# Kernel optimization log

Measured on AMD Instinct MI355X. Metric: run time of the kernel, lower is better.

The kernel has to match this reference:

```python
import jax, jax.numpy as jnp
import numpy as np

B, S, H = 32, 2048, 1024

def setup_inputs() -> dict:
    key = jax.random.key(0)
    ks = jax.random.split(key, 8)
    s = 1.0 / np.sqrt(H)
    return {
        "query": jax.random.normal(ks[0], (B, 1, H), jnp.float32),
        "keys": jax.random.normal(ks[1], (B, S, H), jnp.float32),
        "Wa_w": jax.random.normal(ks[2], (H, H), jnp.float32) * s,
        "Wa_b": jax.random.normal(ks[3], (H,), jnp.float32) * s,
        "Ua_w": jax.random.normal(ks[4], (H, H), jnp.float32) * s,
        "Ua_b": jax.random.normal(ks[5], (H,), jnp.float32) * s,
        "Va_w": jax.random.normal(ks[6], (1, H), jnp.float32) * s,
        "Va_b": jax.random.normal(ks[7], (1,), jnp.float32) * s,
    }

def reference(query, keys, Wa_w, Wa_b, Ua_w, Ua_b, Va_w, Va_b):
    # Wa(query): (B,1,H); Ua(keys): (B,S,H); broadcast add -> (B,S,H)
    q = jnp.einsum('bqh,oh->bqo', query, Wa_w) + Wa_b
    k = jnp.einsum('bsh,oh->bso', keys, Ua_w) + Ua_b
    h = jnp.tanh(q + k)                              # (B,S,H)
    scores = jnp.einsum('bsh,oh->bso', h, Va_w) + Va_b  # (B,S,1)
    scores = scores[:, :, 0][:, None, :]             # (B,1,S)
    weights = jax.nn.softmax(scores, axis=-1)        # (B,1,S)
    context = jnp.einsum('bqs,bsh->bqh', weights, keys)  # (B,1,H)
    return context, weights
```

## Files before the change

kernel.cpp:

```cpp
#include <hip/hip_runtime.h>
#include <hip/hip_bf16.h>

#define HDIM 1024
#define SEQ  2048
#define BATCH 32
#define M_TOTAL (BATCH * SEQ)
#define BM 256
#define BN 256
#define BK 32
#define KSTEPS (HDIM / BK)
#define NSLICE 16

typedef __bf16 bf16x8 __attribute__((ext_vector_type(8)));
typedef float  f32x4  __attribute__((ext_vector_type(4)));
typedef unsigned short u16;
#define AS1 __attribute__((address_space(1)))
#define AS3 __attribute__((address_space(3)))

__device__ __forceinline__ u16 f2bf(float f) {
    unsigned int u = __float_as_uint(f);
    u += 0x7FFFu + ((u >> 16) & 1u);
    return (u16)(u >> 16);
}

__global__ __launch_bounds__(256) void cvt_kernel(const float* __restrict__ in,
                                                  u16* __restrict__ out) {
    size_t i = ((size_t)blockIdx.x * 256 + threadIdx.x) * 8;
    float4 f0 = *(const float4*)(in + i);
    float4 f1 = *(const float4*)(in + i + 4);
    uint4 v;
    v.x = (unsigned)f2bf(f0.x) | ((unsigned)f2bf(f0.y) << 16);
    v.y = (unsigned)f2bf(f0.z) | ((unsigned)f2bf(f0.w) << 16);
    v.z = (unsigned)f2bf(f1.x) | ((unsigned)f2bf(f1.y) << 16);
    v.w = (unsigned)f2bf(f1.z) | ((unsigned)f2bf(f1.w) << 16);
    *(uint4*)(out + i) = v;
}

__global__ __launch_bounds__(256) void qb_kernel(const float* __restrict__ query,
                                                 const float* __restrict__ Wa_w,
                                                 const float* __restrict__ Wa_b,
                                                 const float* __restrict__ Ua_b,
                                                 float* __restrict__ qb) {
    __shared__ float qs[HDIM];
    const int b = blockIdx.x;
    const int tid = threadIdx.x;
    ((float4*)qs)[tid] = ((const float4*)(query + b * HDIM))[tid];
    __syncthreads();
    const int lane = tid & 63;
    const int w = tid >> 6;
    const int obase = blockIdx.y * 64 + w * 16;
    for (int i = 0; i < 16; i++) {
        int o = obase + i;
        const float4* wrow = (const float4*)(Wa_w + (size_t)o * HDIM);
        float s = 0.f;
        #pragma unroll
        for (int j = 0; j < 4; j++) {
            float4 wv = wrow[j * 64 + lane];
            float4 qv = ((const float4*)qs)[j * 64 + lane];
            s += wv.x * qv.x + wv.y * qv.y + wv.z * qv.z + wv.w * qv.w;
        }
        #pragma unroll
        for (int m = 1; m < 64; m <<= 1) s += __shfl_xor(s, m);
        if (lane == 0) qb[b * HDIM + o] = s + Wa_b[o] + Ua_b[o];
    }
}

#define DSREAD(dst, base, imm) \
    asm volatile("ds_read_b128 %0, %1 offset:" #imm : "=v"(dst) : "v"(base))

#define MFMA4(mi, av, b0v, b1v, b2v, b3v) \
    acc[mi][0] = __builtin_amdgcn_mfma_f32_16x16x32_bf16(av, b0v, acc[mi][0], 0, 0, 0); \
    acc[mi][1] = __builtin_amdgcn_mfma_f32_16x16x32_bf16(av, b1v, acc[mi][1], 0, 0, 0); \
    acc[mi][2] = __builtin_amdgcn_mfma_f32_16x16x32_bf16(av, b2v, acc[mi][2], 0, 0, 0); \
    acc[mi][3] = __builtin_amdgcn_mfma_f32_16x16x32_bf16(av, b3v, acc[mi][3], 0, 0, 0);

__global__ __launch_bounds__(512, 2) void gemm_score_kernel(const u16* __restrict__ keysb,
                                                            const u16* __restrict__ uab,
                                                            const float* __restrict__ qb,
                                                            const float* __restrict__ vaw,
                                                            float* __restrict__ sp) {
    __shared__ __align__(16) u16 As[4][BM * BK];
    __shared__ __align__(16) u16 Bs[4][BN * BK];

    const int tid  = threadIdx.x;
    const int lane = tid & 63;
    const int w    = tid >> 6;
    const int wm   = w >> 2;
    const int wn   = w & 3;

    const int bid = blockIdx.y * 4 + blockIdx.x;
    const int swz = (bid & 7) * 128 + (bid >> 3);
    const int bx  = swz & 3;
    const int by  = swz >> 2;
    const int n0  = bx * BN;
    const int m0  = by * BM;

    const int srow = lane >> 2;
    const int cs   = (lane & 3) ^ ((lane >> 3) & 3);
    const u16* gA0 = keysb + (size_t)(m0 + w * 32 + srow) * HDIM + cs * 8;
    const u16* gB0 = uab   + (size_t)(n0 + w * 32 + srow) * HDIM + cs * 8;
    const int ldst = w * 32 * BK;

    const int fr = lane & 15;
    const int fq = lane >> 4;
    const int sA = fq ^ ((fr >> 1) & 3);
    const unsigned aB0 = (unsigned)(unsigned long long)(const AS3 u16*)&As[0][0]
                       + (unsigned)(((wm * 128 + fr) * BK + sA * 8) * 2);
    const unsigned bB0 = (unsigned)(unsigned long long)(const AS3 u16*)&Bs[0][0]
                       + (unsigned)(((wn * 64  + fr) * BK + sA * 8) * 2);

    f32x4 acc[8][4] = {};

#define STAGE_A(kt) { \
    u16* d = &As[(kt) & 3][ldst]; \
    __builtin_amdgcn_global_load_lds((AS1 void*)(gA0 + (size_t)(kt) * BK), (AS3 void*)d, 16, 0, 0); \
    __builtin_amdgcn_global_load_lds((AS1 void*)(gA0 + (size_t)(kt) * BK + 16 * HDIM), (AS3 void*)(d + 16 * BK), 16, 0, 0); }
#define STAGE_B(kt) { \
    u16* d = &Bs[(kt) & 3][ldst]; \
    __builtin_amdgcn_global_load_lds((AS1 void*)(gB0 + (size_t)(kt) * BK), (AS3 void*)d, 16, 0, 0); \
    __builtin_amdgcn_global_load_lds((AS1 void*)(gB0 + (size_t)(kt) * BK + 16 * HDIM), (AS3 void*)(d + 16 * BK), 16, 0, 0); }

    bf16x8 a0, a1, a2, a3, a4, a5, a6, a7;
    bf16x8 bA0, bA1, bA2, bA3, bB0v, bB1v, bB2v, bB3v;

    STAGE_A(0) STAGE_B(0)
    STAGE_A(1) STAGE_B(1)
    STAGE_A(2) STAGE_B(2)
    asm volatile("s_waitcnt vmcnt(4)" ::: "memory");
    __builtin_amdgcn_s_barrier();
    DSREAD(a0, aB0, 0);    DSREAD(a1, aB0, 1024);
    DSREAD(a2, aB0, 2048); DSREAD(a3, aB0, 3072);
    DSREAD(bA0, bB0, 0);    DSREAD(bA1, bB0, 1024);
    DSREAD(bA2, bB0, 2048); DSREAD(bA3, bB0, 3072);

#define TILE(t, bc0, bc1, bc2, bc3, bn0, bn1, bn2, bn3) { \
    const unsigned at = aB0 + (((t) & 3) << 14);              \
     \
    if ((t) + 3 < KSTEPS) STAGE_A((t) + 3) \
    DSREAD(a4, at, 4096); DSREAD(a5, at, 5120); \
    DSREAD(a6, at, 6144); DSREAD(a7, at, 7168); \
    asm volatile("s_waitcnt lgkmcnt(4)" ::: "memory");        \
    __builtin_amdgcn_sched_barrier(0); \
    __builtin_amdgcn_s_setprio(1); \
    MFMA4(0, a0, bc0, bc1, bc2, bc3) \
    MFMA4(1, a1, bc0, bc1, bc2, bc3) \
    MFMA4(2, a2, bc0, bc1, bc2, bc3) \
    MFMA4(3, a3, bc0, bc1, bc2, bc3) \
    __builtin_amdgcn_s_setprio(0); \
     \
    if ((t) + 3 < KSTEPS) STAGE_B((t) + 3) \
    if ((t) + 1 < KSTEPS) { \
        const unsigned an = aB0 + ((((t) + 1) & 3) << 14); \
        const unsigned bn = bB0 + ((((t) + 1) & 3) << 14); \
        DSREAD(a0, an, 0);    DSREAD(a1, an, 1024); \
        DSREAD(a2, an, 2048); DSREAD(a3, an, 3072); \
        DSREAD(bn0, bn, 0);    DSREAD(bn1, bn, 1024); \
        DSREAD(bn2, bn, 2048); DSREAD(bn3, bn, 3072); \
        asm volatile("s_waitcnt lgkmcnt(8)" ::: "memory");    \
    } else { \
        asm volatile("s_waitcnt lgkmcnt(0)" ::: "memory"); \
    } \
    __builtin_amdgcn_sched_barrier(0); \
    __builtin_amdgcn_s_setprio(1); \
    MFMA4(4, a4, bc0, bc1, bc2, bc3) \
    MFMA4(5, a5, bc0, bc1, bc2, bc3) \
    MFMA4(6, a6, bc0, bc1, bc2, bc3) \
    MFMA4(7, a7, bc0, bc1, bc2, bc3) \
    __builtin_amdgcn_s_setprio(0); \
     \
    if ((t) + 1 < KSTEPS - 2) asm volatile("s_waitcnt vmcnt(4)" ::: "memory"); \
    else                      asm volatile("s_waitcnt vmcnt(0)" ::: "memory"); \
    __builtin_amdgcn_s_barrier(); \
}

    for (int t = 0; t < KSTEPS; t += 2) {
        TILE(t,     bA0, bA1, bA2, bA3, bB0v, bB1v, bB2v, bB3v)
        TILE(t + 1, bB0v, bB1v, bB2v, bB3v, bA0, bA1, bA2, bA3)
    }
#undef TILE
#undef STAGE_A
#undef STAGE_B

    const int bidx = m0 >> 11;
    float qv[4], vv[4];
    #pragma unroll
    for (int ni = 0; ni < 4; ni++) {
        int n_g = n0 + wn * 64 + ni * 16 + fr;
        qv[ni] = qb[bidx * HDIM + n_g];
        vv[ni] = vaw[n_g];
    }
    const int slice = bx * 4 + wn;
    float* sl = sp + ((size_t)slice * BATCH + bidx) * SEQ;
    #pragma unroll
    for (int mi = 0; mi < 8; mi++) {
        #pragma unroll
        for (int r = 0; r < 4; r++) {
            float p = 0.f;
            #pragma unroll
            for (int ni = 0; ni < 4; ni++) {
                float x = acc[mi][ni][r] + qv[ni];
                float e = __expf(2.f * x);
                p += (1.f - 2.f / (e + 1.f)) * vv[ni];
            }
            p += __shfl_xor(p, 1);
            p += __shfl_xor(p, 2);
            p += __shfl_xor(p, 4);
            p += __shfl_xor(p, 8);
            if (fr == 0) {
                int s_g = (m0 + wm * 128 + mi * 16 + fq * 4 + r) & (SEQ - 1);
                sl[s_g] = p;
            }
        }
    }
}

__global__ __launch_bounds__(256) void softmax_kernel(const float* __restrict__ sp,
                                                      float* __restrict__ weights,
                                                      float* __restrict__ ctx) {
    __shared__ float red[4];
    const int b = blockIdx.x;
    const int tid = threadIdx.x;
    float4 z = {0.f, 0.f, 0.f, 0.f};
    ((float4*)(ctx + b * HDIM))[tid] = z;
    float v[8];
    float mx = -1e30f;
    #pragma unroll
    for (int i = 0; i < 8; i++) {
        int s = tid + i * 256;
        float a = 0.f;
        #pragma unroll
        for (int j = 0; j < NSLICE; j++) a += sp[((size_t)j * BATCH + b) * SEQ + s];
        v[i] = a;
        mx = fmaxf(mx, a);
    }
    #pragma unroll
    for (int m = 1; m < 64; m <<= 1) mx = fmaxf(mx, __shfl_xor(mx, m));
    if ((tid & 63) == 0) red[tid >> 6] = mx;
    __syncthreads();
    mx = fmaxf(fmaxf(red[0], red[1]), fmaxf(red[2], red[3]));
    float sum = 0.f;
    #pragma unroll
    for (int i = 0; i < 8; i++) { v[i] = __expf(v[i] - mx); sum += v[i]; }
    #pragma unroll
    for (int m = 1; m < 64; m <<= 1) sum += __shfl_xor(sum, m);
    __syncthreads();
    if ((tid & 63) == 0) red[tid >> 6] = sum;
    __syncthreads();
    sum = red[0] + red[1] + red[2] + red[3];
    float inv = 1.f / sum;
    #pragma unroll
    for (int i = 0; i < 8; i++) weights[b * SEQ + tid + i * 256] = v[i] * inv;
}

__global__ __launch_bounds__(256) void context_kernel(const u16* __restrict__ keysb,
                                                      const float* __restrict__ weights,
                                                      float* __restrict__ ctx) {
    __shared__ float wsm[256];
    const int b = blockIdx.x;
    const int s0 = blockIdx.y * 256;
    const int tid = threadIdx.x;
    wsm[tid] = weights[b * SEQ + s0 + tid];
    __syncthreads();
    const int hq = tid & 127;
    const int sh = (tid >> 7) * 128;
    float a0 = 0.f, a1 = 0.f, a2 = 0.f, a3 = 0.f;
    float a4 = 0.f, a5 = 0.f, a6 = 0.f, a7 = 0.f;
    const uint4* kp = (const uint4*)(keysb + (size_t)b * SEQ * HDIM
                                     + (size_t)(s0 + sh) * HDIM) + hq;
    #pragma unroll 8
    for (int s = 0; s < 128; s++) {
        uint4 kv = kp[s * 128];
        float wv = wsm[sh + s];
        a0 += wv * __uint_as_float(kv.x << 16);
        a1 += wv * __uint_as_float(kv.x & 0xFFFF0000u);
        a2 += wv * __uint_as_float(kv.y << 16);
        a3 += wv * __uint_as_float(kv.y & 0xFFFF0000u);
        a4 += wv * __uint_as_float(kv.z << 16);
        a5 += wv * __uint_as_float(kv.z & 0xFFFF0000u);
        a6 += wv * __uint_as_float(kv.w << 16);
        a7 += wv * __uint_as_float(kv.w & 0xFFFF0000u);
    }
    float* o = ctx + b * HDIM + hq * 8;
    atomicAdd(o + 0, a0);
    atomicAdd(o + 1, a1);
    atomicAdd(o + 2, a2);
    atomicAdd(o + 3, a3);
    atomicAdd(o + 4, a4);
    atomicAdd(o + 5, a5);
    atomicAdd(o + 6, a6);
    atomicAdd(o + 7, a7);
}

extern "C" void kernel_launch(void* const* d_in, const int* in_sizes, int n_in,
                              void* d_out, int out_size, void* d_ws, size_t ws_size,
                              hipStream_t stream) {
    const float* query = (const float*)d_in[0];
    const float* keys  = (const float*)d_in[1];
    const float* Wa_w  = (const float*)d_in[2];
    const float* Wa_b  = (const float*)d_in[3];
    const float* Ua_w  = (const float*)d_in[4];
    const float* Ua_b  = (const float*)d_in[5];
    const float* Va_w  = (const float*)d_in[6];
    float* out = (float*)d_out;

    char* ws = (char*)d_ws;
    u16*  keysb = (u16*)ws;
    u16*  uab   = (u16*)(ws + 134217728);
    float* qb   = (float*)(ws + 134217728 + 2097152);
    float* sp   = (float*)(ws + 134217728 + 2097152 + 131072);

    cvt_kernel<<<(BATCH * SEQ * HDIM) / 2048, 256, 0, stream>>>(keys, keysb);
    cvt_kernel<<<(HDIM * HDIM) / 2048, 256, 0, stream>>>(Ua_w, uab);
    qb_kernel<<<dim3(BATCH, HDIM / 64), 256, 0, stream>>>(query, Wa_w, Wa_b, Ua_b, qb);
    gemm_score_kernel<<<dim3(HDIM / BN, M_TOTAL / BM), 512, 0, stream>>>(keysb, uab, qb, Va_w, sp);
    softmax_kernel<<<BATCH, 256, 0, stream>>>(sp, out + BATCH * HDIM, out);
    context_kernel<<<dim3(BATCH, 8), 256, 0, stream>>>(keysb, out + BATCH * HDIM, out);
}
```

Measured before the change: 598.6 us.

## Load GEMM B fragments directly from global, widen softmax/context blocks, grid-stride convert

```diff
diff --git a/kernel.cpp b/kernel.cpp
--- a/kernel.cpp
+++ b/kernel.cpp
@@ -24,16 +24,19 @@
 }
 
 __global__ __launch_bounds__(256) void cvt_kernel(const float* __restrict__ in,
-                                                  u16* __restrict__ out) {
-    size_t i = ((size_t)blockIdx.x * 256 + threadIdx.x) * 8;
-    float4 f0 = *(const float4*)(in + i);
-    float4 f1 = *(const float4*)(in + i + 4);
-    uint4 v;
-    v.x = (unsigned)f2bf(f0.x) | ((unsigned)f2bf(f0.y) << 16);
-    v.y = (unsigned)f2bf(f0.z) | ((unsigned)f2bf(f0.w) << 16);
-    v.z = (unsigned)f2bf(f1.x) | ((unsigned)f2bf(f1.y) << 16);
-    v.w = (unsigned)f2bf(f1.z) | ((unsigned)f2bf(f1.w) << 16);
-    *(uint4*)(out + i) = v;
+                                                  u16* __restrict__ out, int n8) {
+    const int stride = gridDim.x * 256;
+    for (int idx = blockIdx.x * 256 + threadIdx.x; idx < n8; idx += stride) {
+        size_t i = (size_t)idx * 8;
+        float4 f0 = *(const float4*)(in + i);
+        float4 f1 = *(const float4*)(in + i + 4);
+        uint4 v;
+        v.x = (unsigned)f2bf(f0.x) | ((unsigned)f2bf(f0.y) << 16);
+        v.y = (unsigned)f2bf(f0.z) | ((unsigned)f2bf(f0.w) << 16);
+        v.z = (unsigned)f2bf(f1.x) | ((unsigned)f2bf(f1.y) << 16);
+        v.w = (unsigned)f2bf(f1.z) | ((unsigned)f2bf(f1.w) << 16);
+        *(uint4*)(out + i) = v;
+    }
 }
 
 __global__ __launch_bounds__(256) void qb_kernel(const float* __restrict__ query,
@@ -68,11 +71,11 @@
 #define DSREAD(dst, base, imm) \
     asm volatile("ds_read_b128 %0, %1 offset:" #imm : "=v"(dst) : "v"(base))
 
-#define MFMA4(mi, av, b0v, b1v, b2v, b3v) \
-    acc[mi][0] = __builtin_amdgcn_mfma_f32_16x16x32_bf16(av, b0v, acc[mi][0], 0, 0, 0); \
-    acc[mi][1] = __builtin_amdgcn_mfma_f32_16x16x32_bf16(av, b1v, acc[mi][1], 0, 0, 0); \
-    acc[mi][2] = __builtin_amdgcn_mfma_f32_16x16x32_bf16(av, b2v, acc[mi][2], 0, 0, 0); \
-    acc[mi][3] = __builtin_amdgcn_mfma_f32_16x16x32_bf16(av, b3v, acc[mi][3], 0, 0, 0);
+#define MFMA4(mi, av, c0, c1, c2, c3) \
+    acc[mi][0] = __builtin_amdgcn_mfma_f32_16x16x32_bf16(av, c0, acc[mi][0], 0, 0, 0); \
+    acc[mi][1] = __builtin_amdgcn_mfma_f32_16x16x32_bf16(av, c1, acc[mi][1], 0, 0, 0); \
+    acc[mi][2] = __builtin_amdgcn_mfma_f32_16x16x32_bf16(av, c2, acc[mi][2], 0, 0, 0); \
+    acc[mi][3] = __builtin_amdgcn_mfma_f32_16x16x32_bf16(av, c3, acc[mi][3], 0, 0, 0);
 
 __global__ __launch_bounds__(512, 2) void gemm_score_kernel(const u16* __restrict__ keysb,
                                                             const u16* __restrict__ uab,
@@ -80,7 +83,6 @@
                                                             const float* __restrict__ vaw,
                                                             float* __restrict__ sp) {
     __shared__ __align__(16) u16 As[4][BM * BK];
-    __shared__ __align__(16) u16 Bs[4][BN * BK];
 
     const int tid  = threadIdx.x;
     const int lane = tid & 63;
@@ -98,7 +100,6 @@
     const int srow = lane >> 2;
     const int cs   = (lane & 3) ^ ((lane >> 3) & 3);
     const u16* gA0 = keysb + (size_t)(m0 + w * 32 + srow) * HDIM + cs * 8;
-    const u16* gB0 = uab   + (size_t)(n0 + w * 32 + srow) * HDIM + cs * 8;
     const int ldst = w * 32 * BK;
 
     const int fr = lane & 15;
@@ -106,8 +107,11 @@
     const int sA = fq ^ ((fr >> 1) & 3);
     const unsigned aB0 = (unsigned)(unsigned long long)(const AS3 u16*)&As[0][0]
                        + (unsigned)(((wm * 128 + fr) * BK + sA * 8) * 2);
-    const unsigned bB0 = (unsigned)(unsigned long long)(const AS3 u16*)&Bs[0][0]
-                       + (unsigned)(((wn * 64  + fr) * BK + sA * 8) * 2);
+    const AS1 u16* gBp0 = (const AS1 u16*)uab
+                        + ((size_t)(n0 + wn * 64 + fr) * HDIM + fq * 8);
+    const AS1 u16* gBp1 = gBp0 + (size_t)16 * HDIM;
+    const AS1 u16* gBp2 = gBp0 + (size_t)32 * HDIM;
+    const AS1 u16* gBp3 = gBp0 + (size_t)48 * HDIM;
 
     f32x4 acc[8][4] = {};
 
@@ -115,71 +119,70 @@
     u16* d = &As[(kt) & 3][ldst]; \
     __builtin_amdgcn_global_load_lds((AS1 void*)(gA0 + (size_t)(kt) * BK), (AS3 void*)d, 16, 0, 0); \
     __builtin_amdgcn_global_load_lds((AS1 void*)(gA0 + (size_t)(kt) * BK + 16 * HDIM), (AS3 void*)(d + 16 * BK), 16, 0, 0); }
-#define STAGE_B(kt) { \
-    u16* d = &Bs[(kt) & 3][ldst]; \
-    __builtin_amdgcn_global_load_lds((AS1 void*)(gB0 + (size_t)(kt) * BK), (AS3 void*)d, 16, 0, 0); \
-    __builtin_amdgcn_global_load_lds((AS1 void*)(gB0 + (size_t)(kt) * BK + 16 * HDIM), (AS3 void*)(d + 16 * BK), 16, 0, 0); }
 
     bf16x8 a0, a1, a2, a3, a4, a5, a6, a7;
-    bf16x8 bA0, bA1, bA2, bA3, bB0v, bB1v, bB2v, bB3v;
-
-    STAGE_A(0) STAGE_B(0)
-    STAGE_A(1) STAGE_B(1)
-    STAGE_A(2) STAGE_B(2)
+    bf16x8 bA0, bA1, bA2, bA3, bB0, bB1, bB2, bB3;
+
+    bA0 = *(const AS1 bf16x8*)(gBp0);
+    bA1 = *(const AS1 bf16x8*)(gBp1);
+    bA2 = *(const AS1 bf16x8*)(gBp2);
+    bA3 = *(const AS1 bf16x8*)(gBp3);
+    STAGE_A(0) STAGE_A(1) STAGE_A(2)
     asm volatile("s_waitcnt vmcnt(4)" ::: "memory");
     __builtin_amdgcn_s_barrier();
     DSREAD(a0, aB0, 0);    DSREAD(a1, aB0, 1024);
     DSREAD(a2, aB0, 2048); DSREAD(a3, aB0, 3072);
-    DSREAD(bA0, bB0, 0);    DSREAD(bA1, bB0, 1024);
-    DSREAD(bA2, bB0, 2048); DSREAD(bA3, bB0, 3072);
-
-#define TILE(t, bc0, bc1, bc2, bc3, bn0, bn1, bn2, bn3) { \
-    const unsigned at = aB0 + (((t) & 3) << 14);              \
+
+#define GTILE(t, c0, c1, c2, c3, d0, d1, d2, d3) { \
+    const unsigned at = aB0 + (((t) & 3) << 14);          \
      \
     if ((t) + 3 < KSTEPS) STAGE_A((t) + 3) \
     DSREAD(a4, at, 4096); DSREAD(a5, at, 5120); \
     DSREAD(a6, at, 6144); DSREAD(a7, at, 7168); \
-    asm volatile("s_waitcnt lgkmcnt(4)" ::: "memory");        \
+    if ((t) + 1 < KSTEPS) { \
+        const size_t toff = (size_t)((t) + 1) * BK; \
+        d0 = *(const AS1 bf16x8*)(gBp0 + toff); \
+        d1 = *(const AS1 bf16x8*)(gBp1 + toff); \
+        d2 = *(const AS1 bf16x8*)(gBp2 + toff); \
+        d3 = *(const AS1 bf16x8*)(gBp3 + toff); \
+    } \
+    asm volatile("s_waitcnt lgkmcnt(4)" ::: "memory");    \
     __builtin_amdgcn_sched_barrier(0); \
     __builtin_amdgcn_s_setprio(1); \
-    MFMA4(0, a0, bc0, bc1, bc2, bc3) \
-    MFMA4(1, a1, bc0, bc1, bc2, bc3) \
-    MFMA4(2, a2, bc0, bc1, bc2, bc3) \
-    MFMA4(3, a3, bc0, bc1, bc2, bc3) \
+    MFMA4(0, a0, c0, c1, c2, c3) \
+    MFMA4(1, a1, c0, c1, c2, c3) \
+    MFMA4(2, a2, c0, c1, c2, c3) \
+    MFMA4(3, a3, c0, c1, c2, c3) \
     __builtin_amdgcn_s_setprio(0); \
      \
-    if ((t) + 3 < KSTEPS) STAGE_B((t) + 3) \
     if ((t) + 1 < KSTEPS) { \
         const unsigned an = aB0 + ((((t) + 1) & 3) << 14); \
-        const unsigned bn = bB0 + ((((t) + 1) & 3) << 14); \
         DSREAD(a0, an, 0);    DSREAD(a1, an, 1024); \
         DSREAD(a2, an, 2048); DSREAD(a3, an, 3072); \
-        DSREAD(bn0, bn, 0);    DSREAD(bn1, bn, 1024); \
-        DSREAD(bn2, bn, 2048); DSREAD(bn3, bn, 3072); \
-        asm volatile("s_waitcnt lgkmcnt(8)" ::: "memory");    \
+        asm volatile("s_waitcnt lgkmcnt(4)" ::: "memory");    \
     } else { \
         asm volatile("s_waitcnt lgkmcnt(0)" ::: "memory"); \
     } \
     __builtin_amdgcn_sched_barrier(0); \
     __builtin_amdgcn_s_setprio(1); \
-    MFMA4(4, a4, bc0, bc1, bc2, bc3) \
-    MFMA4(5, a5, bc0, bc1, bc2, bc3) \
-    MFMA4(6, a6, bc0, bc1, bc2, bc3) \
-    MFMA4(7, a7, bc0, bc1, bc2, bc3) \
+    MFMA4(4, a4, c0, c1, c2, c3) \
+    MFMA4(5, a5, c0, c1, c2, c3) \
+    MFMA4(6, a6, c0, c1, c2, c3) \
+    MFMA4(7, a7, c0, c1, c2, c3) \
     __builtin_amdgcn_s_setprio(0); \
      \
-    if ((t) + 1 < KSTEPS - 2) asm volatile("s_waitcnt vmcnt(4)" ::: "memory"); \
-    else                      asm volatile("s_waitcnt vmcnt(0)" ::: "memory"); \
-    __builtin_amdgcn_s_barrier(); \
+    if ((t) < KSTEPS - 3)       asm volatile("s_waitcnt vmcnt(6)" ::: "memory"); \
+    else if ((t) == KSTEPS - 3) asm volatile("s_waitcnt vmcnt(4)" ::: "memory"); \
+    else if ((t) == KSTEPS - 2) asm volatile("s_waitcnt vmcnt(0)" ::: "memory"); \
+    if ((t) < KSTEPS - 1) __builtin_amdgcn_s_barrier(); \
 }
 
     for (int t = 0; t < KSTEPS; t += 2) {
-        TILE(t,     bA0, bA1, bA2, bA3, bB0v, bB1v, bB2v, bB3v)
-        TILE(t + 1, bB0v, bB1v, bB2v, bB3v, bA0, bA1, bA2, bA3)
-    }
-#undef TILE
+        GTILE(t,     bA0, bA1, bA2, bA3, bB0, bB1, bB2, bB3)
+        GTILE(t + 1, bB0, bB1, bB2, bB3, bA0, bA1, bA2, bA3)
+    }
+#undef GTILE
 #undef STAGE_A
-#undef STAGE_B
 
     const int bidx = m0 >> 11;
     float qv[4], vv[4];
@@ -214,61 +217,61 @@
     }
 }
 
-__global__ __launch_bounds__(256) void softmax_kernel(const float* __restrict__ sp,
+__global__ __launch_bounds__(512) void softmax_kernel(const float* __restrict__ sp,
                                                       float* __restrict__ weights,
                                                       float* __restrict__ ctx) {
-    __shared__ float red[4];
+    __shared__ float red[8];
     const int b = blockIdx.x;
     const int tid = threadIdx.x;
-    float4 z = {0.f, 0.f, 0.f, 0.f};
-    ((float4*)(ctx + b * HDIM))[tid] = z;
-    float v[8];
-    float mx = -1e30f;
-    #pragma unroll
-    for (int i = 0; i < 8; i++) {
-        int s = tid + i * 256;
-        float a = 0.f;
-        #pragma unroll
-        for (int j = 0; j < NSLICE; j++) a += sp[((size_t)j * BATCH + b) * SEQ + s];
-        v[i] = a;
-        mx = fmaxf(mx, a);
-    }
+    float2 z2 = {0.f, 0.f};
+    ((float2*)(ctx + b * HDIM))[tid] = z2;
+    const int s = tid * 4;
+    float4 v = {0.f, 0.f, 0.f, 0.f};
+    #pragma unroll
+    for (int j = 0; j < NSLICE; j++) {
+        float4 x = *(const float4*)(sp + ((size_t)j * BATCH + b) * SEQ + s);
+        v.x += x.x; v.y += x.y; v.z += x.z; v.w += x.w;
+    }
+    float mx = fmaxf(fmaxf(v.x, v.y), fmaxf(v.z, v.w));
     #pragma unroll
     for (int m = 1; m < 64; m <<= 1) mx = fmaxf(mx, __shfl_xor(mx, m));
     if ((tid & 63) == 0) red[tid >> 6] = mx;
     __syncthreads();
-    mx = fmaxf(fmaxf(red[0], red[1]), fmaxf(red[2], red[3]));
-    float sum = 0.f;
-    #pragma unroll
-    for (int i = 0; i < 8; i++) { v[i] = __expf(v[i] - mx); sum += v[i]; }
+    mx = fmaxf(fmaxf(fmaxf(red[0], red[1]), fmaxf(red[2], red[3])),
+               fmaxf(fmaxf(red[4], red[5]), fmaxf(red[6], red[7])));
+    v.x = __expf(v.x - mx); v.y = __expf(v.y - mx);
+    v.z = __expf(v.z - mx); v.w = __expf(v.w - mx);
+    float sum = v.x + v.y + v.z + v.w;
     #pragma unroll
     for (int m = 1; m < 64; m <<= 1) sum += __shfl_xor(sum, m);
     __syncthreads();
     if ((tid & 63) == 0) red[tid >> 6] = sum;
     __syncthreads();
-    sum = red[0] + red[1] + red[2] + red[3];
+    sum = (red[0] + red[1]) + (red[2] + red[3]) + (red[4] + red[5]) + (red[6] + red[7]);
     float inv = 1.f / sum;
-    #pragma unroll
-    for (int i = 0; i < 8; i++) weights[b * SEQ + tid + i * 256] = v[i] * inv;
-}
-
-__global__ __launch_bounds__(256) void context_kernel(const u16* __restrict__ keysb,
+    v.x *= inv; v.y *= inv; v.z *= inv; v.w *= inv;
+    *(float4*)(weights + b * SEQ + s) = v;
+}
+
+__global__ __launch_bounds__(512) void context_kernel(const u16* __restrict__ keysb,
                                                       const float* __restrict__ weights,
                                                       float* __restrict__ ctx) {
     __shared__ float wsm[256];
+    __shared__ float part[2][128][9];
     const int b = blockIdx.x;
     const int s0 = blockIdx.y * 256;
     const int tid = threadIdx.x;
-    wsm[tid] = weights[b * SEQ + s0 + tid];
+    if (tid < 256) wsm[tid] = weights[b * SEQ + s0 + tid];
     __syncthreads();
     const int hq = tid & 127;
-    const int sh = (tid >> 7) * 128;
+    const int sq = tid >> 7;
+    const int sh = sq * 64;
     float a0 = 0.f, a1 = 0.f, a2 = 0.f, a3 = 0.f;
     float a4 = 0.f, a5 = 0.f, a6 = 0.f, a7 = 0.f;
     const uint4* kp = (const uint4*)(keysb + (size_t)b * SEQ * HDIM
                                      + (size_t)(s0 + sh) * HDIM) + hq;
     #pragma unroll 8
-    for (int s = 0; s < 128; s++) {
+    for (int s = 0; s < 64; s++) {
         uint4 kv = kp[s * 128];
         float wv = wsm[sh + s];
         a0 += wv * __uint_as_float(kv.x << 16);
@@ -280,15 +283,24 @@
         a6 += wv * __uint_as_float(kv.w << 16);
         a7 += wv * __uint_as_float(kv.w & 0xFFFF0000u);
     }
-    float* o = ctx + b * HDIM + hq * 8;
-    atomicAdd(o + 0, a0);
-    atomicAdd(o + 1, a1);
-    atomicAdd(o + 2, a2);
-    atomicAdd(o + 3, a3);
-    atomicAdd(o + 4, a4);
-    atomicAdd(o + 5, a5);
-    atomicAdd(o + 6, a6);
-    atomicAdd(o + 7, a7);
+    if (sq >= 2) {
+        float* p = part[sq - 2][hq];
+        p[0] = a0; p[1] = a1; p[2] = a2; p[3] = a3;
+        p[4] = a4; p[5] = a5; p[6] = a6; p[7] = a7;
+    }
+    __syncthreads();
+    if (sq < 2) {
+        const float* p = part[sq][hq];
+        float* o = ctx + b * HDIM + hq * 8;
+        atomicAdd(o + 0, a0 + p[0]);
+        atomicAdd(o + 1, a1 + p[1]);
+        atomicAdd(o + 2, a2 + p[2]);
+        atomicAdd(o + 3, a3 + p[3]);
+        atomicAdd(o + 4, a4 + p[4]);
+        atomicAdd(o + 5, a5 + p[5]);
+        atomicAdd(o + 6, a6 + p[6]);
+        atomicAdd(o + 7, a7 + p[7]);
+    }
 }
 
 extern "C" void kernel_launch(void* const* d_in, const int* in_sizes, int n_in,
@@ -309,10 +321,10 @@
     float* qb   = (float*)(ws + 134217728 + 2097152);
     float* sp   = (float*)(ws + 134217728 + 2097152 + 131072);
 
-    cvt_kernel<<<(BATCH * SEQ * HDIM) / 2048, 256, 0, stream>>>(keys, keysb);
-    cvt_kernel<<<(HDIM * HDIM) / 2048, 256, 0, stream>>>(Ua_w, uab);
+    cvt_kernel<<<2048, 256, 0, stream>>>(keys, keysb, BATCH * SEQ * HDIM / 8);
+    cvt_kernel<<<512, 256, 0, stream>>>(Ua_w, uab, HDIM * HDIM / 8);
     qb_kernel<<<dim3(BATCH, HDIM / 64), 256, 0, stream>>>(query, Wa_w, Wa_b, Ua_b, qb);
     gemm_score_kernel<<<dim3(HDIM / BN, M_TOTAL / BM), 512, 0, stream>>>(keysb, uab, qb, Va_w, sp);
-    softmax_kernel<<<BATCH, 256, 0, stream>>>(sp, out + BATCH * HDIM, out);
-    context_kernel<<<dim3(BATCH, 8), 256, 0, stream>>>(keysb, out + BATCH * HDIM, out);
-}
+    softmax_kernel<<<BATCH, 512, 0, stream>>>(sp, out + BATCH * HDIM, out);
+    context_kernel<<<dim3(BATCH, 8), 512, 0, stream>>>(keysb, out + BATCH * HDIM, out);
+}
```

New measurement: 688.1 us. 15.0% more time.
